# Kernel tuning notes

Measured on AMD Instinct MI355X. Metric: run time of the kernel, lower is better.

## Reference

```python
import jax, jax.numpy as jnp
import numpy as np

N_NODES = 50000
N_EDGES = 800000
HID = 256
HEADS = 4
HEAD_C = HID // HEADS  # 64
IN_CH = 16
OUT_CH = 4
NEG_SLOPE = 0.2  # PyG GATConv default LeakyReLU slope
LN_EPS = 1e-5


def setup_inputs() -> dict:
    key = jax.random.key(0)
    ks = jax.random.split(key, 12)
    s = 0.05
    return {
        "x": jax.random.normal(ks[0], (N_NODES, IN_CH), dtype=jnp.float32),
        "edge_index": jax.random.randint(ks[1], (2, N_EDGES), 0, N_NODES, dtype=jnp.int64),
        "w_in": jax.random.normal(ks[2], (IN_CH, HID), dtype=jnp.float32) * s,
        "b_in": jnp.zeros((HID,), dtype=jnp.float32),
        "w_gat": jax.random.normal(ks[3], (4, HID, HID), dtype=jnp.float32) * s,
        "att_src": jax.random.normal(ks[4], (4, HEADS, HEAD_C), dtype=jnp.float32) * s,
        "att_dst": jax.random.normal(ks[5], (4, HEADS, HEAD_C), dtype=jnp.float32) * s,
        "b_gat": jnp.zeros((4, HID), dtype=jnp.float32),
        "ln_scale": jnp.ones((4, HID), dtype=jnp.float32),
        "ln_bias": jnp.zeros((4, HID), dtype=jnp.float32),
        "w_out": jax.random.normal(ks[6], (HID, OUT_CH), dtype=jnp.float32) * s,
        "b_out": jnp.zeros((OUT_CH,), dtype=jnp.float32),
    }


def _gat_layer(x, src, dst, W, a_src, a_dst, bias, g, beta):
    """One GATConv(concat, heads=4) + LayerNorm + ELU. x:[N,HID]."""
    n = x.shape[0]
    h = (x @ W).reshape(n, HEADS, HEAD_C)                 # [N,H,C]
    a_s = jnp.einsum("nhc,hc->nh", h, a_src)              # [N,H]
    a_d = jnp.einsum("nhc,hc->nh", h, a_dst)              # [N,H]
    logits = jax.nn.leaky_relu(a_s[src] + a_d[dst], NEG_SLOPE)  # [E,H]
    # segment softmax over destination neighborhoods (self-loops ensure non-empty)
    m = jax.ops.segment_max(logits, dst, num_segments=n)
    e = jnp.exp(logits - m[dst])
    denom = jax.ops.segment_sum(e, dst, num_segments=n)
    alpha = e / (denom[dst] + 1e-16)                      # [E,H]
    msg = alpha[:, :, None] * h[src]                      # [E,H,C]
    out = jax.ops.segment_sum(msg, dst, num_segments=n).reshape(n, HID) + bias
    mu = out.mean(-1, keepdims=True)
    var = out.var(-1, keepdims=True)
    out = (out - mu) * jax.lax.rsqrt(var + LN_EPS) * g + beta
    return jax.nn.elu(out)


def reference(x, edge_index, w_in, b_in, w_gat, att_src, att_dst, b_gat,
              ln_scale, ln_bias, w_out, b_out):
    n = x.shape[0]
    # PyG GATConv adds self-loops by default
    loops = jnp.arange(n, dtype=edge_index.dtype)
    ei = jnp.concatenate([edge_index, jnp.stack([loops, loops])], axis=1)
    src, dst = ei[0], ei[1]

    x = x @ w_in + b_in                                   # input_proj
    h = x
    for l in (0, 1):
        h = _gat_layer(h, src, dst, w_gat[l], att_src[l], att_dst[l],
                       b_gat[l], ln_scale[l], ln_bias[l])
    x = x + h
    h = x
    for l in (2, 3):
        h = _gat_layer(h, src, dst, w_gat[l], att_src[l], att_dst[l],
                       b_gat[l], ln_scale[l], ln_bias[l])
    x = x + h
    return x @ w_out + b_out
```

## Files before the change

kernel.cpp:

```cpp
#include <hip/hip_runtime.h>
#include <math.h>

#define NN 50000
#define E0 800000
#define ET 850000
#define HID 256
#define INCH 16
#define MAXDEG 64

#define NB_Z    49
#define NB_WT   256
#define NB_IP   6250
#define NB_PREP (NB_Z + NB_WT + NB_IP)

#define NB_G    782
#define NB_EDGE 3321
#define NB_G0   (NB_G + NB_EDGE)

typedef _Float16 h8 __attribute__((ext_vector_type(8)));
typedef float f32x4 __attribute__((ext_vector_type(4)));

__device__ __forceinline__ void load_lds16(const void* g, void* l) {
    __builtin_amdgcn_global_load_lds(
        (const __attribute__((address_space(1))) unsigned int*)g,
        (__attribute__((address_space(3))) unsigned int*)l, 16, 0, 0);
}

__global__ __launch_bounds__(256) void prep_kernel(
    int* __restrict__ cursor,
    const float* __restrict__ w_gat, _Float16* __restrict__ WT,
    const float* __restrict__ x, const float* __restrict__ w_in,
    const float* __restrict__ b_in, _Float16* __restrict__ Ph) {
    int b = blockIdx.x, t = threadIdx.x;
    if (b < NB_Z) {
        int i = (b * 256 + t) * 4;
#pragma unroll
        for (int k = 0; k < 4; ++k)
            if (i + k < NN) cursor[i + k] = 0;
    } else if (b < NB_Z + NB_WT) {
        int k = b - NB_Z;
#pragma unroll
        for (int l = 0; l < 4; ++l) {
            float v = w_gat[((size_t)l * 256 + k) * 256 + t];
            WT[((size_t)l * 256 + t) * 256 + k] = (_Float16)v;
        }
    } else {
        int ipb = b - NB_Z - NB_WT;
        int sub = t >> 5, l32 = t & 31;
        int n = ipb * 8 + sub;
        int c0 = l32 * 8;
        const float* xr = x + n * INCH;
        float a[8];
#pragma unroll
        for (int k = 0; k < 8; k += 4) {
            float4 bb = *(const float4*)(b_in + c0 + k);
            a[k] = bb.x; a[k + 1] = bb.y; a[k + 2] = bb.z; a[k + 3] = bb.w;
        }
#pragma unroll
        for (int k = 0; k < INCH; ++k) {
            float xv = xr[k];
            const float4 w0 = *(const float4*)(w_in + k * 256 + c0);
            const float4 w1 = *(const float4*)(w_in + k * 256 + c0 + 4);
            a[0] += xv * w0.x; a[1] += xv * w0.y; a[2] += xv * w0.z; a[3] += xv * w0.w;
            a[4] += xv * w1.x; a[5] += xv * w1.y; a[6] += xv * w1.z; a[7] += xv * w1.w;
        }
        h8 o;
#pragma unroll
        for (int k = 0; k < 8; ++k) o[k] = (_Float16)a[k];
        *(h8*)(Ph + (size_t)n * 256 + c0) = o;
    }
}

__device__ __forceinline__ void gemm_tile(
    int rb, int cb,
    const _Float16* __restrict__ A, const _Float16* __restrict__ BT,
    _Float16* __restrict__ H, const float* __restrict__ att_s,
    const float* __restrict__ att_d, float* __restrict__ AS, float* __restrict__ AD,
    _Float16* As, _Float16* Bs) {
    int t = threadIdx.x;
    int wv = t >> 6, lane = t & 63;
    int wr = (wv >> 1) * 64, wc = (wv & 1) * 64;
    int lm = lane & 15, lq = lane >> 4;
    f32x4 acc[4][4] = {};

    int rch = lane >> 2;
    int q = lane & 3;

    for (int k0 = 0; k0 < 256; k0 += 32) {
#pragma unroll
        for (int c = 0; c < 2; ++c) {
            int r = wv * 32 + c * 16 + rch;
            int g = q ^ ((r >> 1) & 3);
            int ra = rb + r; if (ra >= NN) ra = NN - 1;
            load_lds16(A + (size_t)ra * 256 + k0 + g * 8,
                       (char*)As + wv * 2048 + c * 1024);
            load_lds16(BT + (size_t)(cb + r) * 256 + k0 + g * 8,
                       (char*)Bs + wv * 2048 + c * 1024);
        }
        __syncthreads();
        h8 af[4], bfr[4];
#pragma unroll
        for (int i = 0; i < 4; ++i) {
            int row = wr + i * 16 + lm;
            af[i] = *(const h8*)((const char*)As + row * 64 + ((lq ^ ((row >> 1) & 3)) * 16));
        }
#pragma unroll
        for (int j = 0; j < 4; ++j) {
            int row = wc + j * 16 + lm;
            bfr[j] = *(const h8*)((const char*)Bs + row * 64 + ((lq ^ ((row >> 1) & 3)) * 16));
        }
#pragma unroll
        for (int i = 0; i < 4; ++i)
#pragma unroll
            for (int j = 0; j < 4; ++j)
                acc[i][j] = __builtin_amdgcn_mfma_f32_16x16x32_f16(af[i], bfr[j], acc[i][j], 0, 0, 0);
        __syncthreads();
    }

    int head = (cb + wc) >> 6;
    float sa[4], sd[4];
#pragma unroll
    for (int j = 0; j < 4; ++j) {
        sa[j] = att_s[head * 64 + j * 16 + lm];
        sd[j] = att_d[head * 64 + j * 16 + lm];
    }
#pragma unroll
    for (int i = 0; i < 4; ++i)
#pragma unroll
        for (int rr = 0; rr < 4; ++rr) {
            float vs = acc[i][0][rr] * sa[0] + acc[i][1][rr] * sa[1]
                     + acc[i][2][rr] * sa[2] + acc[i][3][rr] * sa[3];
            float vd = acc[i][0][rr] * sd[0] + acc[i][1][rr] * sd[1]
                     + acc[i][2][rr] * sd[2] + acc[i][3][rr] * sd[3];
#pragma unroll
            for (int o = 1; o <= 8; o <<= 1) {
                vs += __shfl_xor(vs, o, 64);
                vd += __shfl_xor(vd, o, 64);
            }
            int row = rb + wr + i * 16 + lq * 4 + rr;
            if (lm == 0 && row < NN) {
                AS[row * 4 + head] = vs;
                AD[row * 4 + head] = vd;
            }
        }

#pragma unroll
    for (int i = 0; i < 4; ++i)
#pragma unroll
        for (int j = 0; j < 4; ++j) {
            int col = cb + wc + j * 16 + lm;
#pragma unroll
            for (int rr = 0; rr < 4; ++rr) {
                int row = rb + wr + i * 16 + lq * 4 + rr;
                if (row < NN) H[(size_t)row * 256 + col] = (_Float16)acc[i][j][rr];
            }
        }
}

__global__ __launch_bounds__(256) void gemm_fused_kernel(
    const _Float16* __restrict__ A, const _Float16* __restrict__ BT,
    _Float16* __restrict__ H, const float* __restrict__ att_s,
    const float* __restrict__ att_d, float* __restrict__ AS, float* __restrict__ AD) {
    __shared__ _Float16 As[128 * 32];
    __shared__ _Float16 Bs[128 * 32];
    gemm_tile(blockIdx.x * 128, blockIdx.y * 128, A, BT, H, att_s, att_d, AS, AD, As, Bs);
}

__global__ __launch_bounds__(256) void gemm0_scatter_kernel(
    const _Float16* __restrict__ A, const _Float16* __restrict__ BT,
    _Float16* __restrict__ H, const float* __restrict__ att_s,
    const float* __restrict__ att_d, float* __restrict__ AS, float* __restrict__ AD,
    const int* __restrict__ ei, int* __restrict__ cursor,
    int* __restrict__ csr_pad) {
    __shared__ _Float16 As[128 * 32];
    __shared__ _Float16 Bs[128 * 32];
    int b = blockIdx.x;
    if (b >= NB_G) {
        int e = (b - NB_G) * 256 + threadIdx.x;
        if (e < ET) {
            int s, d;
            if (e < E0) { s = ei[e]; d = ei[E0 + e]; }
            else        { s = d = e - E0; }
            int pos = atomicAdd(&cursor[d], 1);
            if (pos < MAXDEG) csr_pad[(d << 6) + pos] = s;
        }
        return;
    }
    gemm_tile((b >> 1) * 128, (b & 1) * 128, A, BT, H, att_s, att_d, AS, AD, As, Bs);
}

__global__ __launch_bounds__(256) void agg_kernel(
    const _Float16* __restrict__ H, const float4* __restrict__ AS,
    const float4* __restrict__ AD,
    const int* __restrict__ cnt, const int* __restrict__ csr_pad,
    const float* __restrict__ bias, const float* __restrict__ g, const float* __restrict__ beta,
    const _Float16* __restrict__ res, _Float16* __restrict__ outh,
    const float* __restrict__ wout, const float* __restrict__ bout,
    float* __restrict__ out) {
    int t = threadIdx.x;
    int l32 = t & 31;
    int n = blockIdx.x * 8 + (t >> 5);
    int deg = cnt[n];
    if (deg > MAXDEG) deg = MAXDEG;
    int start = n << 6, end = start + deg;
    float4 adv = AD[n];
    int head = l32 >> 3;
    int c0 = l32 * 8;
    float advh = (head == 0) ? adv.x : (head == 1) ? adv.y : (head == 2) ? adv.z : adv.w;

    float acc[8] = {};
    float acc_e = 0.f;
#pragma unroll 4
    for (int i = start; i < end; ++i) {
        int s = csr_pad[i];
        const float* as = (const float*)&AS[s];
        float v = as[head] + advh;
        v = (v >= 0.f) ? v : 0.2f * v;
        float e = __expf(v);
        acc_e += e;
        h8 hv = *(const h8*)(H + (size_t)s * 256 + c0);
#pragma unroll
        for (int k = 0; k < 8; ++k) acc[k] += e * (float)hv[k];
    }
    float dinv = 1.f / (acc_e + 1e-16f);

    float val[8];
#pragma unroll
    for (int k = 0; k < 8; k += 4) {
        float4 bb = *(const float4*)(bias + c0 + k);
        val[k]     = acc[k]     * dinv + bb.x;
        val[k + 1] = acc[k + 1] * dinv + bb.y;
        val[k + 2] = acc[k + 2] * dinv + bb.z;
        val[k + 3] = acc[k + 3] * dinv + bb.w;
    }

    float s1 = 0.f, s2 = 0.f;
#pragma unroll
    for (int k = 0; k < 8; ++k) { s1 += val[k]; s2 += val[k] * val[k]; }
#pragma unroll
    for (int o = 16; o >= 1; o >>= 1) {
        s1 += __shfl_xor(s1, o, 64);
        s2 += __shfl_xor(s2, o, 64);
    }
    float mu = s1 * (1.f / 256.f);
    float var = s2 * (1.f / 256.f) - mu * mu;
    float rs = rsqrtf(var + 1e-5f);

    float y[8];
#pragma unroll
    for (int k = 0; k < 8; k += 4) {
        float4 g4 = *(const float4*)(g + c0 + k);
        float4 b4 = *(const float4*)(beta + c0 + k);
        y[k]     = (val[k]     - mu) * rs * g4.x + b4.x;
        y[k + 1] = (val[k + 1] - mu) * rs * g4.y + b4.y;
        y[k + 2] = (val[k + 2] - mu) * rs * g4.z + b4.z;
        y[k + 3] = (val[k + 3] - mu) * rs * g4.w + b4.w;
    }
#pragma unroll
    for (int k = 0; k < 8; ++k) y[k] = (y[k] > 0.f) ? y[k] : (__expf(y[k]) - 1.f);
    if (res) {
        h8 r0 = *(const h8*)(res + (size_t)n * 256 + c0);
#pragma unroll
        for (int k = 0; k < 8; ++k) y[k] += (float)r0[k];
    }
    if (wout) {
        float o0 = 0.f, o1 = 0.f, o2 = 0.f, o3 = 0.f;
#pragma unroll
        for (int k = 0; k < 8; ++k) {
            float4 wv = *(const float4*)(wout + (size_t)(c0 + k) * 4);
            o0 += y[k] * wv.x; o1 += y[k] * wv.y; o2 += y[k] * wv.z; o3 += y[k] * wv.w;
        }
#pragma unroll
        for (int o = 16; o >= 1; o >>= 1) {
            o0 += __shfl_xor(o0, o, 64);
            o1 += __shfl_xor(o1, o, 64);
            o2 += __shfl_xor(o2, o, 64);
            o3 += __shfl_xor(o3, o, 64);
        }
        if (l32 == 0) {
            float4 ov = make_float4(o0 + bout[0], o1 + bout[1], o2 + bout[2], o3 + bout[3]);
            *(float4*)(out + (size_t)n * 4) = ov;
        }
    } else {
        h8 o0;
#pragma unroll
        for (int k = 0; k < 8; ++k) o0[k] = (_Float16)y[k];
        *(h8*)(outh + (size_t)n * 256 + c0) = o0;
    }
}

extern "C" void kernel_launch(void* const* d_in, const int* in_sizes, int n_in,
                              void* d_out, int out_size, void* d_ws, size_t ws_size,
                              hipStream_t stream) {
    const float* x       = (const float*)d_in[0];
    const int*   ei      = (const int*)  d_in[1];
    const float* w_in    = (const float*)d_in[2];
    const float* b_in    = (const float*)d_in[3];
    const float* w_gat   = (const float*)d_in[4];
    const float* att_src = (const float*)d_in[5];
    const float* att_dst = (const float*)d_in[6];
    const float* b_gat   = (const float*)d_in[7];
    const float* ln_g    = (const float*)d_in[8];
    const float* ln_b    = (const float*)d_in[9];
    const float* w_out   = (const float*)d_in[10];
    const float* b_out   = (const float*)d_in[11];
    float* out = (float*)d_out;

    char* ws = (char*)d_ws;
    size_t off = 0;
    auto alloc = [&](size_t bytes) {
        void* p = ws + off;
        off += (bytes + 255) & ~(size_t)255;
        return p;
    };
    _Float16*  Ph      = (_Float16*)alloc((size_t)NN * HID * 2);
    _Float16*  Ch      = (_Float16*)alloc((size_t)NN * HID * 2);
    _Float16*  Gh      = (_Float16*)alloc((size_t)NN * HID * 2);
    _Float16*  H       = (_Float16*)alloc((size_t)NN * HID * 2);
    _Float16*  WT      = (_Float16*)alloc((size_t)4 * HID * HID * 2);
    float*     ASAD    = (float*)alloc((size_t)NN * 8 * 4);
    int*       cursor  = (int*)alloc((size_t)NN * 4);
    int*       csr_pad = (int*)alloc((size_t)NN * MAXDEG * 4);

    float* AS = ASAD;
    float* AD = ASAD + (size_t)NN * 4;

    const dim3 GEMM_GRID(391, 2);
    const int NB_AGG = NN / 8;

    prep_kernel<<<NB_PREP, 256, 0, stream>>>(cursor, w_gat, WT, x, w_in, b_in, Ph);

    gemm0_scatter_kernel<<<NB_G0, 256, 0, stream>>>(
        Ph, WT, H, att_src, att_dst, AS, AD, ei, cursor, csr_pad);
    agg_kernel<<<NB_AGG, 256, 0, stream>>>(
        H, (const float4*)AS, (const float4*)AD, cursor, csr_pad,
        b_gat, ln_g, ln_b, nullptr, Gh, nullptr, nullptr, nullptr);

    auto run_layer = [&](const _Float16* inh, int l, const _Float16* res, _Float16* outh,
                         const float* wo, const float* bo) {
        gemm_fused_kernel<<<GEMM_GRID, 256, 0, stream>>>(
            inh, WT + (size_t)l * HID * HID, H,
            att_src + l * 256, att_dst + l * 256, AS, AD);
        agg_kernel<<<NB_AGG, 256, 0, stream>>>(
            H, (const float4*)AS, (const float4*)AD, cursor, csr_pad,
            b_gat + l * 256, ln_g + l * 256, ln_b + l * 256, res, outh, wo, bo,
            wo ? out : nullptr);
    };

    run_layer(Gh, 1, Ph,      Ch, nullptr, nullptr);
    run_layer(Ch, 2, nullptr, Gh, nullptr, nullptr);
    run_layer(Gh, 3, Ch,      Ph, w_out,   b_out);
}
```

Baseline: 527.6 us.

## Preload full B tile into LDS once and stream A fragments from global

The GEMM tile now loads the whole 128x256 weight block into LDS (64KB) up front with an XOR swizzle, then runs the k-loop with no per-iteration barriers. A fragments are read directly from global memory into registers instead of being staged through LDS. This removes eight rounds of barrier synchronization and the LDS staging for A. In exchange, LDS use per block grows, which may reduce occupancy, and A loads hit global memory with less coalesced access. The gemm0 scatter blocks also now reserve 64KB of LDS even though they do not use it.

Result: slower. 538.4 us (+2.1%).

```diff
diff --git a/kernel.cpp b/kernel.cpp
--- a/kernel.cpp
+++ b/kernel.cpp
@@ -76,45 +76,51 @@
     const _Float16* __restrict__ A, const _Float16* __restrict__ BT,
     _Float16* __restrict__ H, const float* __restrict__ att_s,
     const float* __restrict__ att_d, float* __restrict__ AS, float* __restrict__ AD,
-    _Float16* As, _Float16* Bs) {
+    _Float16* Bs ) {
     int t = threadIdx.x;
     int wv = t >> 6, lane = t & 63;
     int wr = (wv >> 1) * 64, wc = (wv & 1) * 64;
     int lm = lane & 15, lq = lane >> 4;
+
+    {
+        int rof = lane >> 5;
+        int pg = lane & 31;
+#pragma unroll
+        for (int pass = 0; pass < 16; ++pass) {
+            int rbase = wv * 2 + pass * 8;
+            int r = rbase + rof;
+            int kg = pg ^ (r & 15);
+            load_lds16(BT + (size_t)(cb + r) * 256 + kg * 8,
+                       (char*)Bs + rbase * 512);
+        }
+    }
+    __syncthreads();
+
+    const _Float16* ap[4];
+#pragma unroll
+    for (int i = 0; i < 4; ++i) {
+        int ra = rb + wr + i * 16 + lm;
+        if (ra >= NN) ra = NN - 1;
+        ap[i] = A + (size_t)ra * 256 + lq * 8;
+    }
+
     f32x4 acc[4][4] = {};
-
-    int rch = lane >> 2;
-    int q = lane & 3;
-
+#pragma unroll 2
     for (int k0 = 0; k0 < 256; k0 += 32) {
-#pragma unroll
-        for (int c = 0; c < 2; ++c) {
-            int r = wv * 32 + c * 16 + rch;
-            int g = q ^ ((r >> 1) & 3);
-            int ra = rb + r; if (ra >= NN) ra = NN - 1;
-            load_lds16(A + (size_t)ra * 256 + k0 + g * 8,
-                       (char*)As + wv * 2048 + c * 1024);
-            load_lds16(BT + (size_t)(cb + r) * 256 + k0 + g * 8,
-                       (char*)Bs + wv * 2048 + c * 1024);
-        }
-        __syncthreads();
         h8 af[4], bfr[4];
 #pragma unroll
-        for (int i = 0; i < 4; ++i) {
-            int row = wr + i * 16 + lm;
-            af[i] = *(const h8*)((const char*)As + row * 64 + ((lq ^ ((row >> 1) & 3)) * 16));
-        }
+        for (int i = 0; i < 4; ++i) af[i] = *(const h8*)(ap[i] + k0);
+        int kg = (k0 >> 3) + lq;
 #pragma unroll
         for (int j = 0; j < 4; ++j) {
             int row = wc + j * 16 + lm;
-            bfr[j] = *(const h8*)((const char*)Bs + row * 64 + ((lq ^ ((row >> 1) & 3)) * 16));
+            bfr[j] = *(const h8*)((const char*)Bs + row * 512 + ((kg ^ (row & 15)) * 16));
         }
 #pragma unroll
         for (int i = 0; i < 4; ++i)
 #pragma unroll
             for (int j = 0; j < 4; ++j)
                 acc[i][j] = __builtin_amdgcn_mfma_f32_16x16x32_f16(af[i], bfr[j], acc[i][j], 0, 0, 0);
-        __syncthreads();
     }
 
     int head = (cb + wc) >> 6;
@@ -161,9 +167,8 @@
     const _Float16* __restrict__ A, const _Float16* __restrict__ BT,
     _Float16* __restrict__ H, const float* __restrict__ att_s,
     const float* __restrict__ att_d, float* __restrict__ AS, float* __restrict__ AD) {
-    __shared__ _Float16 As[128 * 32];
-    __shared__ _Float16 Bs[128 * 32];
-    gemm_tile(blockIdx.x * 128, blockIdx.y * 128, A, BT, H, att_s, att_d, AS, AD, As, Bs);
+    __shared__ _Float16 Bs[128 * 256];
+    gemm_tile(blockIdx.x * 128, blockIdx.y * 128, A, BT, H, att_s, att_d, AS, AD, Bs);
 }
 
 __global__ __launch_bounds__(256) void gemm0_scatter_kernel(
@@ -172,8 +177,7 @@
     const float* __restrict__ att_d, float* __restrict__ AS, float* __restrict__ AD,
     const int* __restrict__ ei, int* __restrict__ cursor,
     int* __restrict__ csr_pad) {
-    __shared__ _Float16 As[128 * 32];
-    __shared__ _Float16 Bs[128 * 32];
+    __shared__ _Float16 Bs[128 * 256];
     int b = blockIdx.x;
     if (b >= NB_G) {
         int e = (b - NB_G) * 256 + threadIdx.x;
@@ -186,7 +190,7 @@
         }
         return;
     }
-    gemm_tile((b >> 1) * 128, (b & 1) * 128, A, BT, H, att_s, att_d, AS, AD, As, Bs);
+    gemm_tile((b >> 1) * 128, (b & 1) * 128, A, BT, H, att_s, att_d, AS, AD, Bs);
 }
 
 __global__ __launch_bounds__(256) void agg_kernel(
```
